# Optimization experiments

Hardware: AMD Instinct MI355X
Metric: run time of the kernel (lower is better)

Reference implementation:

```python
import jax, jax.numpy as jnp
import numpy as np

B, C, H, W, NH = 8, 192, 128, 128, 6  # batch, channels, height, width, heads


def setup_inputs() -> dict:
    key = jax.random.key(0)
    ks = jax.random.split(key, 5)
    return {
        "x": jax.random.normal(ks[0], (B, C, H, W), jnp.float32),
        "w_qkv": jax.random.normal(ks[1], (3 * C, 1, 3, 3), jnp.float32) * 0.1,  # grouped conv, groups=C
        "b_qkv": jax.random.normal(ks[2], (3 * C,), jnp.float32) * 0.1,
        "temperature": jnp.ones((NH, 1, 1), jnp.float32),
        "w_out": jax.random.normal(ks[3], (C, C), jnp.float32) * 0.05,  # 1x1 conv as dense
        "b_out": jax.random.normal(ks[4], (C,), jnp.float32) * 0.05,
    }


def reference(x, w_qkv, b_qkv, temperature, w_out, b_out):
    b, c, h, w = x.shape
    nh = temperature.shape[0]
    # grouped 3x3 conv (groups = in_ch), padding=1
    qkv = jax.lax.conv_general_dilated(
        x, w_qkv, window_strides=(1, 1), padding=[(1, 1), (1, 1)],
        feature_group_count=c, dimension_numbers=("NCHW", "OIHW", "NCHW"),
    ) + b_qkv[None, :, None, None]
    q, k, v = jnp.split(qkv, 3, axis=1)  # each [b, c, h, w]

    def to_heads(t):
        return t.reshape(b, nh, c // nh, h * w)  # b head c (h w)

    q, k, v = to_heads(q), to_heads(k), to_heads(v)
    eps = 1e-12  # F.normalize default
    q = q / jnp.maximum(jnp.linalg.norm(q, axis=-1, keepdims=True), eps)
    k = k / jnp.maximum(jnp.linalg.norm(k, axis=-1, keepdims=True), eps)
    attn = jnp.einsum("bhcn,bhdn->bhcd", q, k) * temperature[None]  # [b, nh, c/nh, c/nh]
    attn = jax.nn.softmax(attn, axis=-1)
    out = jnp.einsum("bhcd,bhdn->bhcn", attn, v).reshape(b, c, h, w)
    out = jnp.einsum("oc,bchw->bohw", w_out, out) + b_out[None, :, None, None]
    return out
```

## Files before the change

kernel.cpp:

```cpp
#include <hip/hip_runtime.h>
#include <hip/hip_bf16.h>

constexpr int B   = 8;
constexpr int Cc  = 192;
constexpr int H   = 128;
constexpr int Wd  = 128;
constexpr int NH  = 6;
constexpr int HD  = 32;
constexpr int HW  = H * Wd;

typedef short s16x8 __attribute__((ext_vector_type(8)));
typedef float f32x16 __attribute__((ext_vector_type(16)));

constexpr size_t OFF_V    = 0;
constexpr size_t OFF_ATTN = 50331648ULL;
constexpr size_t OFF_SSQ  = OFF_ATTN + 196608ULL;
constexpr size_t OFF_ZERO = OFF_SSQ + 12288ULL;
constexpr size_t OFF_M    = OFF_ZERO + 256ULL;
constexpr int    N_ZERO   = (196608 + 12288 + 256) / 4;

__device__ inline unsigned short f2bf(float f) {
    __hip_bfloat16 h = __float2bfloat16(f);
    return *(unsigned short*)&h;
}

__global__ void zero_kernel(float* __restrict__ p, int n) {
    int i = blockIdx.x * 256 + threadIdx.x;
    if (i < n) p[i] = 0.f;
}

#define AS1C(p) ((const __attribute__((address_space(1))) void*)(p))
#define AS3(p)  ((__attribute__((address_space(3))) void*)(p))


__device__ __forceinline__ void ld6(const float* __restrict__ base, int r,
                                    int q8, float (&e)[6]) {
    const float* p = base + r * 40 + q8 * 4;
    float4 a = *(const float4*)p;
    float4 bq = *(const float4*)(p + 4);
    float2 cd = *(const float2*)(p + 8);
    e[0] = a.w; e[1] = bq.x; e[2] = bq.y; e[3] = bq.z; e[4] = bq.w; e[5] = cd.x;
}

__device__ __forceinline__ float conv_lds(
    const float* __restrict__ base, const float (&wr)[9], float br,
    int q8, int ch, unsigned short* __restrict__ frag)
{
    float rv[3][6];
    ld6(base, 0, q8, rv[0]);
    ld6(base, 1, q8, rv[1]);
    float ss = 0.f;
#pragma unroll
    for (int y = 0; y < 4; ++y) {
        ld6(base, y + 2, q8, rv[(y + 2) % 3]);
        const float* r0 = rv[y % 3];
        const float* r1 = rv[(y + 1) % 3];
        const float* r2 = rv[(y + 2) % 3];
        float o[4];
#pragma unroll
        for (int xx = 0; xx < 4; ++xx) {
            o[xx] = br
                + wr[0] * r0[xx] + wr[1] * r0[xx + 1] + wr[2] * r0[xx + 2]
                + wr[3] * r1[xx] + wr[4] * r1[xx + 1] + wr[5] * r1[xx + 2]
                + wr[6] * r2[xx] + wr[7] * r2[xx + 1] + wr[8] * r2[xx + 2];
        }
        ss += o[0] * o[0] + o[1] * o[1] + o[2] * o[2] + o[3] * o[3];
        ushort4 pk = make_ushort4(f2bf(o[0]), f2bf(o[1]), f2bf(o[2]), f2bf(o[3]));
        int g = 4 * y + (q8 >> 1);
        *(ushort4*)(frag + ((g * 32 + ch) << 3) + ((q8 & 1) << 2)) = pk;
    }
    return ss;
}

__global__ __launch_bounds__(256, 2) void fused_conv_qk(
    const float* __restrict__ x, const float* __restrict__ w,
    const float* __restrict__ bias, float* __restrict__ ssq,
    float* __restrict__ attn, const float* __restrict__ zbuf)
{
    const int tile = blockIdx.x, h = blockIdx.y, b = blockIdx.z;
    const int y0  = tile * 4;
    const int tid = threadIdx.x;
    const int ch  = tid >> 3, q8 = tid & 7;
    const int lane = tid & 63, wv = tid >> 6;
    const int m = lane & 31, hf = lane >> 5;

    __shared__ float xs[2][5760];
    __shared__ unsigned short qs[16 * 32 * 8];
    __shared__ unsigned short ks[16 * 32 * 8];

    const int gq0 = (h * 32) / 3;
    const int ncq = (h * 32 + 31) / 3 - gq0 + 1;
    const int gl  = (h * 32 + ch) / 3 - gq0;

    const int ocq = h * HD + ch;
    float wq[9], wk[9];
#pragma unroll
    for (int t = 0; t < 9; ++t) {
        wq[t] = w[(size_t)ocq * 9 + t];
        wk[t] = w[(size_t)(Cc + ocq) * 9 + t];
    }
    const float bq = bias[ocq], bk = bias[Cc + ocq];

    const float* sp[6];
    int cb[6];
    int i4[6];
    bool act[6];
#pragma unroll
    for (int j = 0; j < 6; ++j) {
        int i = tid + 256 * j;
        act[j] = (i < 1440);
        if (act[j]) {
            int t   = i / 720;
            int jj  = i - t * 720;
            int c   = jj / 60;
            int rem = jj - c * 60;
            int r   = rem / 10;
            int c4  = rem - r * 10;
            int cg  = (c < ncq) ? c : (ncq - 1);
            int gch = t * 64 + gq0 + cg;
            int y   = y0 - 1 + r;
            sp[j] = (y >= 0 && y < H)
                  ? x + ((size_t)b * Cc + gch) * HW + (size_t)y * Wd : nullptr;
            cb[j] = c4 * 4 - 4;
            i4[j] = i * 4;
        } else { sp[j] = nullptr; cb[j] = 0; i4[j] = 0; }
    }

    f32x16 acc;
#pragma unroll
    for (int i = 0; i < 16; ++i) acc[i] = 0.f;
    float ssq_a = 0.f, ssk_a = 0.f;

#pragma unroll
    for (int j = 0; j < 6; ++j) {
        if (!act[j]) continue;
        int col = cb[j];
        const float* src = (sp[j] != nullptr && (unsigned)col <= 124u)
                         ? sp[j] + col : zbuf;
        __builtin_amdgcn_global_load_lds(AS1C(src), AS3(&xs[0][i4[j]]), 16, 0, 0);
    }

#pragma unroll 1
    for (int s = 0; s < 4; ++s) {
        float* cur = xs[s & 1];
        __syncthreads();

        if (s < 3) {
            float* nxt = xs[(s + 1) & 1];
#pragma unroll
            for (int j = 0; j < 6; ++j) {
                if (!act[j]) continue;
                int col = (s + 1) * 32 + cb[j];
                const float* src = (sp[j] != nullptr && (unsigned)col <= 124u)
                                 ? sp[j] + col : zbuf;
                __builtin_amdgcn_global_load_lds(AS1C(src), AS3(&nxt[i4[j]]), 16, 0, 0);
            }
        }

        ssq_a += conv_lds(cur + gl * 240, wq, bq, q8, ch, qs);
        ssk_a += conv_lds(cur + 2880 + gl * 240, wk, bk, q8, ch, ks);
        __syncthreads();

#pragma unroll
        for (int cc = 0; cc < 2; ++cc) {
            int g = (wv * 2 + cc) * 2 + hf;
            s16x8 qa = *(const s16x8*)&qs[(g * 32 + m) << 3];
            s16x8 kb = *(const s16x8*)&ks[(g * 32 + m) << 3];
            acc = __builtin_amdgcn_mfma_f32_32x32x16_bf16(qa, kb, acc, 0, 0, 0);
        }
    }

    __syncthreads();
    float* sacc = (float*)qs;
    for (int i = tid; i < 1024; i += 256) sacc[i] = 0.f;
    __syncthreads();
#pragma unroll
    for (int r = 0; r < 16; ++r) {
        int row = (r & 3) + 8 * (r >> 2) + 4 * hf;
        atomicAdd(&sacc[row * 32 + m], acc[r]);
    }
    __syncthreads();
    float* ap = attn + (size_t)(b * NH + h) * 1024;
    for (int i = tid; i < 1024; i += 256) atomicAdd(&ap[i], sacc[i]);

    for (int off = 4; off; off >>= 1) {
        ssq_a += __shfl_down(ssq_a, off, 8);
        ssk_a += __shfl_down(ssk_a, off, 8);
    }
    if (q8 == 0) {
        atomicAdd(&ssq[b * Cc + ocq], ssq_a);
        atomicAdd(&ssq[B * Cc + b * Cc + ocq], ssk_a);
    }
}

constexpr int TS = 16;

__global__ __launch_bounds__(256) void conv_v(
    const float* __restrict__ x, const float* __restrict__ w,
    const float* __restrict__ bias, unsigned short* __restrict__ vws)
{
    int tile = blockIdx.x;
    int gv   = blockIdx.y;
    int b    = blockIdx.z;
    int y0   = tile * TS;

    __shared__ float sm[TS + 2][132];

    const float* xp = x + ((size_t)b * Cc + 128 + gv) * HW;
    for (int i = threadIdx.x; i < (TS + 2) * 32; i += 256) {
        int r = i >> 5, c4 = (i & 31) * 4;
        int y = y0 - 1 + r;
        if (y >= 0 && y < H) {
            float4 v4 = *(const float4*)(xp + (size_t)y * Wd + c4);
            sm[r][c4 + 1] = v4.x; sm[r][c4 + 2] = v4.y;
            sm[r][c4 + 3] = v4.z; sm[r][c4 + 4] = v4.w;
        } else {
            sm[r][c4 + 1] = 0.f; sm[r][c4 + 2] = 0.f;
            sm[r][c4 + 3] = 0.f; sm[r][c4 + 4] = 0.f;
        }
    }
    for (int i = threadIdx.x; i < (TS + 2) * 2; i += 256) {
        int r = i >> 1;
        sm[r][(i & 1) ? 129 : 0] = 0.f;
    }
    __syncthreads();

    float wreg[3][9], breg[3];
    for (int j = 0; j < 3; ++j) {
        const float* wp = w + (size_t)(2 * Cc + 3 * gv + j) * 9;
#pragma unroll
        for (int t = 0; t < 9; ++t) wreg[j][t] = wp[t];
        breg[j] = bias[2 * Cc + 3 * gv + j];
    }

    int xq = (threadIdx.x & 31) * 4;
    int ys = threadIdx.x >> 5;

    for (int yy = ys; yy < TS; yy += 8) {
        float rvv[3][6];
        for (int r = 0; r < 3; ++r) {
            float4 a4 = *(const float4*)&sm[yy + r][xq];
            float2 a2 = *(const float2*)&sm[yy + r][xq + 4];
            rvv[r][0] = a4.x; rvv[r][1] = a4.y; rvv[r][2] = a4.z;
            rvv[r][3] = a4.w; rvv[r][4] = a2.x; rvv[r][5] = a2.y;
        }
        for (int j = 0; j < 3; ++j) {
            unsigned short pk[4];
            for (int xx = 0; xx < 4; ++xx) {
                float s = breg[j]
                    + wreg[j][0] * rvv[0][xx] + wreg[j][1] * rvv[0][xx + 1] + wreg[j][2] * rvv[0][xx + 2]
                    + wreg[j][3] * rvv[1][xx] + wreg[j][4] * rvv[1][xx + 1] + wreg[j][5] * rvv[1][xx + 2]
                    + wreg[j][6] * rvv[2][xx] + wreg[j][7] * rvv[2][xx + 1] + wreg[j][8] * rvv[2][xx + 2];
                pk[xx] = f2bf(s);
            }
            unsigned short* op = vws + ((size_t)b * Cc + 3 * gv + j) * HW
                                     + (size_t)(y0 + yy) * Wd + xq;
            *(ushort4*)op = make_ushort4(pk[0], pk[1], pk[2], pk[3]);
        }
    }
}

__global__ void softmax_attn(float* __restrict__ attn,
                             const float* __restrict__ ssq,
                             const float* __restrict__ temp)
{
    int h = blockIdx.x % NH, b = blockIdx.x / NH;
    __shared__ float nk[32];
    if (threadIdx.x < 32)
        nk[threadIdx.x] = fmaxf(sqrtf(ssq[B * Cc + b * Cc + h * 32 + threadIdx.x]), 1e-12f);
    __syncthreads();
    int c = threadIdx.x;
    if (c >= 32) return;
    float nq = fmaxf(sqrtf(ssq[b * Cc + h * 32 + c]), 1e-12f);
    float t = temp[h];
    float* ap = attn + ((size_t)(b * NH + h) * 32 + c) * 32;
    float row[32];
    float mx = -1e30f;
    for (int d = 0; d < 32; ++d) {
        float v = ap[d] / (nq * nk[d]) * t;
        row[d] = v;
        mx = fmaxf(mx, v);
    }
    float sum = 0.f;
    for (int d = 0; d < 32; ++d) { row[d] = expf(row[d] - mx); sum += row[d]; }
    float inv = 1.f / sum;
    for (int d = 0; d < 32; ++d) ap[d] = row[d] * inv;
}

__global__ __launch_bounds__(256) void make_m(
    const float* __restrict__ attn, const float* __restrict__ w_out,
    unsigned short* __restrict__ M)
{
    int h = blockIdx.x, b = blockIdx.y;
    __shared__ float as[32][33];
    for (int i = threadIdx.x; i < 1024; i += 256)
        as[i / 32][i % 32] = attn[(size_t)((b * NH + h) * 32 + i / 32) * 32 + i % 32];
    __syncthreads();
    for (int i = threadIdx.x; i < Cc * 32; i += 256) {
        int o = i / 32, d = i % 32;
        const float* wp = w_out + (size_t)o * Cc + h * 32;
        float s = 0.f;
        for (int cp = 0; cp < 32; ++cp) s += wp[cp] * as[cp][d];
        M[((size_t)b * Cc + o) * Cc + h * 32 + d] = f2bf(s);
    }
}

constexpr int BN = 128;

__global__ __launch_bounds__(256) void out_gemm(
    const unsigned short* __restrict__ vws, const unsigned short* __restrict__ M,
    const float* __restrict__ b_out, float* __restrict__ out)
{
    int n0 = blockIdx.x * BN;
    int b  = blockIdx.y;

    const unsigned short* vp = vws + (size_t)b * Cc * HW;
    const unsigned short* mp = M + (size_t)b * Cc * Cc;

    __shared__ unsigned short vsT[BN][24];

    int tid  = threadIdx.x;
    int lane = tid & 63, wv = tid >> 6;
    int wm = wv & 1, wn = wv >> 1;
    int col = lane & 31, half = lane >> 5;

    f32x16 acc[6];
    for (int t = 0; t < 6; ++t)
        for (int i = 0; i < 16; ++i) acc[t][i] = 0.f;

    int p  = tid >> 5;
    int nq = tid & 31;

    const unsigned short* s0 = vp + (size_t)(2 * p) * HW + n0 + 4 * nq;
    ushort4 va = *(const ushort4*)s0;
    ushort4 vb = *(const ushort4*)(s0 + HW);

    for (int k0 = 0; k0 < Cc; k0 += 16) {
        *(unsigned int*)&vsT[4 * nq + 0][2 * p] = (unsigned int)va.x | ((unsigned int)vb.x << 16);
        *(unsigned int*)&vsT[4 * nq + 1][2 * p] = (unsigned int)va.y | ((unsigned int)vb.y << 16);
        *(unsigned int*)&vsT[4 * nq + 2][2 * p] = (unsigned int)va.z | ((unsigned int)vb.z << 16);
        *(unsigned int*)&vsT[4 * nq + 3][2 * p] = (unsigned int)va.w | ((unsigned int)vb.w << 16);
        __syncthreads();

        ushort4 va2 = make_ushort4(0, 0, 0, 0), vb2 = va2;
        if (k0 + 16 < Cc) {
            const unsigned short* s1 = vp + (size_t)(k0 + 16 + 2 * p) * HW + n0 + 4 * nq;
            va2 = *(const ushort4*)s1;
            vb2 = *(const ushort4*)(s1 + HW);
        }

        s16x8 af[3], bf[2];
        for (int mt = 0; mt < 3; ++mt) {
            int o = wm * 96 + mt * 32 + col;
            af[mt] = *(const s16x8*)(mp + (size_t)o * Cc + k0 + half * 8);
        }
        for (int nt = 0; nt < 2; ++nt) {
            int nn = wn * 64 + nt * 32 + col;
            bf[nt] = *(const s16x8*)&vsT[nn][half * 8];
        }
        for (int mt = 0; mt < 3; ++mt)
            for (int nt = 0; nt < 2; ++nt)
                acc[mt * 2 + nt] = __builtin_amdgcn_mfma_f32_32x32x16_bf16(
                    af[mt], bf[nt], acc[mt * 2 + nt], 0, 0, 0);
        __syncthreads();
        va = va2; vb = vb2;
    }

    for (int mt = 0; mt < 3; ++mt)
        for (int nt = 0; nt < 2; ++nt) {
            f32x16 c = acc[mt * 2 + nt];
            int n = n0 + wn * 64 + nt * 32 + col;
            for (int r = 0; r < 16; ++r) {
                int row = (r & 3) + 8 * (r >> 2) + 4 * half;
                int o = wm * 96 + mt * 32 + row;
                out[((size_t)b * Cc + o) * HW + n] = c[r] + b_out[o];
            }
        }
}

extern "C" void kernel_launch(void* const* d_in, const int* in_sizes, int n_in,
                              void* d_out, int out_size, void* d_ws, size_t ws_size,
                              hipStream_t stream) {
    const float* x      = (const float*)d_in[0];
    const float* w_qkv  = (const float*)d_in[1];
    const float* b_qkv  = (const float*)d_in[2];
    const float* temp   = (const float*)d_in[3];
    const float* w_out  = (const float*)d_in[4];
    const float* b_out  = (const float*)d_in[5];
    float* out = (float*)d_out;

    char* ws = (char*)d_ws;
    unsigned short* vws = (unsigned short*)(ws + OFF_V);
    float* attn         = (float*)(ws + OFF_ATTN);
    float* ssq          = (float*)(ws + OFF_SSQ);
    const float* zbuf   = (const float*)(ws + OFF_ZERO);
    unsigned short* M   = (unsigned short*)(ws + OFF_M);

    zero_kernel<<<(N_ZERO + 255) / 256, 256, 0, stream>>>(attn, N_ZERO);
    fused_conv_qk<<<dim3(H / 4, NH, B), 256, 0, stream>>>(x, w_qkv, b_qkv, ssq, attn, zbuf);
    conv_v<<<dim3(H / TS, 64, B), 256, 0, stream>>>(x, w_qkv, b_qkv, vws);
    softmax_attn<<<B * NH, 64, 0, stream>>>(attn, ssq, temp);
    make_m<<<dim3(NH, B), 256, 0, stream>>>(attn, w_out, M);
    out_gemm<<<dim3(HW / BN, B), 256, 0, stream>>>(vws, M, b_out, out);
}
```

Baseline: 292.7 us.

## Split QK conv across column strips and coalesce out_gemm stores via LDS

The fused conv+QK kernel no longer loops over four 32-column strips with double-buffered LDS. Each block now handles a single strip, giving four times as many blocks with a single-buffered LDS tile, and occupancy is raised to 4 blocks per CU. This adds more atomic reductions into attn and ssq. In out_gemm, the M fragments are prefetched one k-step ahead, and the output tile is staged through per-wave LDS so stores become coalesced float4 writes instead of scattered scalar stores.

After: 369.2 us. 26.2% more time.

```diff
diff --git a/kernel.cpp b/kernel.cpp
--- a/kernel.cpp
+++ b/kernel.cpp
@@ -72,19 +72,21 @@
     return ss;
 }
 
-__global__ __launch_bounds__(256, 2) void fused_conv_qk(
+__global__ __launch_bounds__(256, 4) void fused_conv_qk(
     const float* __restrict__ x, const float* __restrict__ w,
     const float* __restrict__ bias, float* __restrict__ ssq,
     float* __restrict__ attn, const float* __restrict__ zbuf)
 {
-    const int tile = blockIdx.x, h = blockIdx.y, b = blockIdx.z;
+    const int bx = blockIdx.x;
+    const int tile = bx >> 2, sidx = bx & 3;
+    const int h = blockIdx.y, b = blockIdx.z;
     const int y0  = tile * 4;
     const int tid = threadIdx.x;
     const int ch  = tid >> 3, q8 = tid & 7;
     const int lane = tid & 63, wv = tid >> 6;
     const int m = lane & 31, hf = lane >> 5;
 
-    __shared__ float xs[2][5760];
+    __shared__ float xs[5760];
     __shared__ unsigned short qs[16 * 32 * 8];
     __shared__ unsigned short ks[16 * 32 * 8];
 
@@ -101,73 +103,40 @@
     }
     const float bq = bias[ocq], bk = bias[Cc + ocq];
 
-    const float* sp[6];
-    int cb[6];
-    int i4[6];
-    bool act[6];
 #pragma unroll
     for (int j = 0; j < 6; ++j) {
         int i = tid + 256 * j;
-        act[j] = (i < 1440);
-        if (act[j]) {
-            int t   = i / 720;
-            int jj  = i - t * 720;
-            int c   = jj / 60;
-            int rem = jj - c * 60;
-            int r   = rem / 10;
-            int c4  = rem - r * 10;
-            int cg  = (c < ncq) ? c : (ncq - 1);
-            int gch = t * 64 + gq0 + cg;
-            int y   = y0 - 1 + r;
-            sp[j] = (y >= 0 && y < H)
-                  ? x + ((size_t)b * Cc + gch) * HW + (size_t)y * Wd : nullptr;
-            cb[j] = c4 * 4 - 4;
-            i4[j] = i * 4;
-        } else { sp[j] = nullptr; cb[j] = 0; i4[j] = 0; }
-    }
+        if (i >= 1440) break;
+        int t   = i / 720;
+        int jj  = i - t * 720;
+        int c   = jj / 60;
+        int rem = jj - c * 60;
+        int r   = rem / 10;
+        int c4  = rem - r * 10;
+        int cg  = (c < ncq) ? c : (ncq - 1);
+        int gch = t * 64 + gq0 + cg;
+        int y   = y0 - 1 + r;
+        int col = sidx * 32 + c4 * 4 - 4;
+        const float* src = (y >= 0 && y < H && (unsigned)col <= 124u)
+            ? x + ((size_t)b * Cc + gch) * HW + (size_t)y * Wd + col
+            : zbuf;
+        __builtin_amdgcn_global_load_lds(AS1C(src), AS3(&xs[i * 4]), 16, 0, 0);
+    }
+    __syncthreads();
+
+    float ssq_a = conv_lds(xs + gl * 240, wq, bq, q8, ch, qs);
+    float ssk_a = conv_lds(xs + 2880 + gl * 240, wk, bk, q8, ch, ks);
+    __syncthreads();
 
     f32x16 acc;
 #pragma unroll
     for (int i = 0; i < 16; ++i) acc[i] = 0.f;
-    float ssq_a = 0.f, ssk_a = 0.f;
-
-#pragma unroll
-    for (int j = 0; j < 6; ++j) {
-        if (!act[j]) continue;
-        int col = cb[j];
-        const float* src = (sp[j] != nullptr && (unsigned)col <= 124u)
-                         ? sp[j] + col : zbuf;
-        __builtin_amdgcn_global_load_lds(AS1C(src), AS3(&xs[0][i4[j]]), 16, 0, 0);
-    }
-
-#pragma unroll 1
-    for (int s = 0; s < 4; ++s) {
-        float* cur = xs[s & 1];
-        __syncthreads();
-
-        if (s < 3) {
-            float* nxt = xs[(s + 1) & 1];
-#pragma unroll
-            for (int j = 0; j < 6; ++j) {
-                if (!act[j]) continue;
-                int col = (s + 1) * 32 + cb[j];
-                const float* src = (sp[j] != nullptr && (unsigned)col <= 124u)
-                                 ? sp[j] + col : zbuf;
-                __builtin_amdgcn_global_load_lds(AS1C(src), AS3(&nxt[i4[j]]), 16, 0, 0);
-            }
-        }
-
-        ssq_a += conv_lds(cur + gl * 240, wq, bq, q8, ch, qs);
-        ssk_a += conv_lds(cur + 2880 + gl * 240, wk, bk, q8, ch, ks);
-        __syncthreads();
-
-#pragma unroll
-        for (int cc = 0; cc < 2; ++cc) {
-            int g = (wv * 2 + cc) * 2 + hf;
-            s16x8 qa = *(const s16x8*)&qs[(g * 32 + m) << 3];
-            s16x8 kb = *(const s16x8*)&ks[(g * 32 + m) << 3];
-            acc = __builtin_amdgcn_mfma_f32_32x32x16_bf16(qa, kb, acc, 0, 0, 0);
-        }
+#pragma unroll
+    for (int cc = 0; cc < 2; ++cc) {
+        int g = (wv * 2 + cc) * 2 + hf;
+        s16x8 qa = *(const s16x8*)&qs[(g * 32 + m) << 3];
+        s16x8 kb = *(const s16x8*)&ks[(g * 32 + m) << 3];
+        acc = __builtin_amdgcn_mfma_f32_32x32x16_bf16(qa, kb, acc, 0, 0, 0);
     }
 
     __syncthreads();
@@ -307,7 +276,7 @@
 
 constexpr int BN = 128;
 
-__global__ __launch_bounds__(256) void out_gemm(
+__global__ __launch_bounds__(256, 2) void out_gemm(
     const unsigned short* __restrict__ vws, const unsigned short* __restrict__ M,
     const float* __restrict__ b_out, float* __restrict__ out)
 {
@@ -318,6 +287,7 @@
     const unsigned short* mp = M + (size_t)b * Cc * Cc;
 
     __shared__ unsigned short vsT[BN][24];
+    __shared__ float cbuf[4][32 * 36];
 
     int tid  = threadIdx.x;
     int lane = tid & 63, wv = tid >> 6;
@@ -325,7 +295,9 @@
     int col = lane & 31, half = lane >> 5;
 
     f32x16 acc[6];
+#pragma unroll
     for (int t = 0; t < 6; ++t)
+#pragma unroll
         for (int i = 0; i < 16; ++i) acc[t][i] = 0.f;
 
     int p  = tid >> 5;
@@ -334,6 +306,12 @@
     const unsigned short* s0 = vp + (size_t)(2 * p) * HW + n0 + 4 * nq;
     ushort4 va = *(const ushort4*)s0;
     ushort4 vb = *(const ushort4*)(s0 + HW);
+    s16x8 af[3];
+#pragma unroll
+    for (int mt = 0; mt < 3; ++mt) {
+        int o = wm * 96 + mt * 32 + col;
+        af[mt] = *(const s16x8*)(mp + (size_t)o * Cc + half * 8);
+    }
 
     for (int k0 = 0; k0 < Cc; k0 += 16) {
         *(unsigned int*)&vsT[4 * nq + 0][2 * p] = (unsigned int)va.x | ((unsigned int)vb.x << 16);
@@ -343,37 +321,60 @@
         __syncthreads();
 
         ushort4 va2 = make_ushort4(0, 0, 0, 0), vb2 = va2;
-        if (k0 + 16 < Cc) {
+        s16x8 af2[3];
+        bool more = (k0 + 16 < Cc);
+        if (more) {
             const unsigned short* s1 = vp + (size_t)(k0 + 16 + 2 * p) * HW + n0 + 4 * nq;
             va2 = *(const ushort4*)s1;
             vb2 = *(const ushort4*)(s1 + HW);
-        }
-
-        s16x8 af[3], bf[2];
-        for (int mt = 0; mt < 3; ++mt) {
-            int o = wm * 96 + mt * 32 + col;
-            af[mt] = *(const s16x8*)(mp + (size_t)o * Cc + k0 + half * 8);
-        }
+#pragma unroll
+            for (int mt = 0; mt < 3; ++mt) {
+                int o = wm * 96 + mt * 32 + col;
+                af2[mt] = *(const s16x8*)(mp + (size_t)o * Cc + k0 + 16 + half * 8);
+            }
+        }
+
+        s16x8 bf[2];
+#pragma unroll
         for (int nt = 0; nt < 2; ++nt) {
             int nn = wn * 64 + nt * 32 + col;
             bf[nt] = *(const s16x8*)&vsT[nn][half * 8];
         }
+#pragma unroll
         for (int mt = 0; mt < 3; ++mt)
+#pragma unroll
             for (int nt = 0; nt < 2; ++nt)
                 acc[mt * 2 + nt] = __builtin_amdgcn_mfma_f32_32x32x16_bf16(
                     af[mt], bf[nt], acc[mt * 2 + nt], 0, 0, 0);
         __syncthreads();
-        va = va2; vb = vb2;
-    }
-
+        if (more) {
+            va = va2; vb = vb2;
+#pragma unroll
+            for (int mt = 0; mt < 3; ++mt) af[mt] = af2[mt];
+        }
+    }
+
+    float* wb = cbuf[wv];
+#pragma unroll
     for (int mt = 0; mt < 3; ++mt)
+#pragma unroll
         for (int nt = 0; nt < 2; ++nt) {
-            f32x16 c = acc[mt * 2 + nt];
-            int n = n0 + wn * 64 + nt * 32 + col;
+#pragma unroll
             for (int r = 0; r < 16; ++r) {
                 int row = (r & 3) + 8 * (r >> 2) + 4 * half;
-                int o = wm * 96 + mt * 32 + row;
-                out[((size_t)b * Cc + o) * HW + n] = c[r] + b_out[o];
+                wb[row * 36 + col] = acc[mt * 2 + nt][r];
+            }
+            int o0 = wm * 96 + mt * 32;
+            int nb = n0 + wn * 64 + nt * 32;
+#pragma unroll
+            for (int it = 0; it < 4; ++it) {
+                int row = (lane >> 3) + 8 * it;
+                int c4  = (lane & 7) * 4;
+                float4 v4 = *(const float4*)&wb[row * 36 + c4];
+                int o = o0 + row;
+                float bo = b_out[o];
+                v4.x += bo; v4.y += bo; v4.z += bo; v4.w += bo;
+                *(float4*)&out[((size_t)b * Cc + o) * HW + nb + c4] = v4;
             }
         }
 }
@@ -397,7 +398,7 @@
     unsigned short* M   = (unsigned short*)(ws + OFF_M);
 
     zero_kernel<<<(N_ZERO + 255) / 256, 256, 0, stream>>>(attn, N_ZERO);
-    fused_conv_qk<<<dim3(H / 4, NH, B), 256, 0, stream>>>(x, w_qkv, b_qkv, ssq, attn, zbuf);
+    fused_conv_qk<<<dim3(128, NH, B), 256, 0, stream>>>(x, w_qkv, b_qkv, ssq, attn, zbuf);
     conv_v<<<dim3(H / TS, 64, B), 256, 0, stream>>>(x, w_qkv, b_qkv, vws);
     softmax_attn<<<B * NH, 64, 0, stream>>>(attn, ssq, temp);
     make_m<<<dim3(NH, B), 256, 0, stream>>>(attn, w_out, M);
```
